# Kernel optimization log

Hardware: AMD Instinct MI355X
Metric: run time of the kernel (lower is better)

Reference implementation:

```python
import jax, jax.numpy as jnp
import numpy as np

NUM_HEADS = 16
HEAD_SIZE = 64
CTXT_LEN = 2048
N_EMBED = 1024
BATCH = 2


def setup_inputs() -> dict:
    key = jax.random.key(0)
    ks = jax.random.split(key, 5)
    s = 0.02  # realistic init scale for weights
    return {
        "x": jax.random.normal(ks[0], (BATCH, CTXT_LEN, N_EMBED), dtype=jnp.float32),
        "Wk": jax.random.normal(ks[1], (N_EMBED, NUM_HEADS * HEAD_SIZE), dtype=jnp.float32) * s,
        "bk": jnp.zeros((NUM_HEADS * HEAD_SIZE,), dtype=jnp.float32),
        "Wq": jax.random.normal(ks[2], (N_EMBED, NUM_HEADS * HEAD_SIZE), dtype=jnp.float32) * s,
        "bq": jnp.zeros((NUM_HEADS * HEAD_SIZE,), dtype=jnp.float32),
        "Wv": jax.random.normal(ks[3], (N_EMBED, NUM_HEADS * HEAD_SIZE), dtype=jnp.float32) * s,
        "bv": jnp.zeros((NUM_HEADS * HEAD_SIZE,), dtype=jnp.float32),
        "Wo": jax.random.normal(ks[4], (NUM_HEADS * HEAD_SIZE, N_EMBED), dtype=jnp.float32) * s,
        "bo": jnp.zeros((N_EMBED,), dtype=jnp.float32),
    }


def reference(x, Wk, bk, Wq, bq, Wv, bv, Wo, bo):
    B, T, E = x.shape
    H, D = NUM_HEADS, HEAD_SIZE
    # QKV projections -> [B, T, H, D]
    k = (x @ Wk + bk).reshape(B, T, H, D)
    q = (x @ Wq + bq).reshape(B, T, H, D)
    v = (x @ Wv + bv).reshape(B, T, H, D)
    # NOTE: source scales by 1/sqrt(n_embed), not 1/sqrt(head_size)
    scale = 1.0 / (E ** 0.5)
    wei = jnp.einsum('bthd,bshd->bhts', q, k) * scale  # [B, H, T, T]
    causal = jnp.tril(jnp.ones((T, T), dtype=bool))
    wei = jnp.where(causal, wei, -jnp.inf)
    wei = jax.nn.softmax(wei, axis=-1)
    # dropout p=0.0 -> identity
    out = jnp.einsum('bhts,bshd->bthd', wei, v).reshape(B, T, H * D)
    return out @ Wo + bo
```

## Files before the change

### kernel.cpp

```cpp
#include <hip/hip_runtime.h>

#define NH 16
#define HS 64
#define T_CTX 2048
#define NE 1024
#define NB 2
#define BT (NB*T_CTX)
#define HD (NH*HS)

typedef unsigned short u16;
typedef __bf16 bf16_t;
typedef bf16_t bf16x8 __attribute__((ext_vector_type(8)));
typedef float f32x4 __attribute__((ext_vector_type(4)));
typedef u16 u16x8 __attribute__((ext_vector_type(8)));
typedef u16 u16x4 __attribute__((ext_vector_type(4)));

#define GLDS(gp, lp) __builtin_amdgcn_global_load_lds( \
    (const __attribute__((address_space(1))) void*)(gp), \
    (__attribute__((address_space(3))) void*)(lp), 16, 0, 0)

__device__ __forceinline__ u16 f2bf(float f) {
  union { float f; unsigned u; } x; x.f = f;
  return (u16)((x.u + 0x7fffu + ((x.u >> 16) & 1u)) >> 16);
}
__device__ __forceinline__ float bf2f(u16 u) {
  union { unsigned u; float f; } x; x.u = ((unsigned)u) << 16;
  return x.f;
}

__global__ __launch_bounds__(256) void k_prep_x(const float* __restrict__ x,
                                                u16* __restrict__ xb) {
  int i = blockIdx.x * blockDim.x + threadIdx.x;
  float4 v = ((const float4*)x)[i];
  ushort4 o;
  o.x = f2bf(v.x); o.y = f2bf(v.y); o.z = f2bf(v.z); o.w = f2bf(v.w);
  ((ushort4*)xb)[i] = o;
}

__global__ __launch_bounds__(256) void k_prep_w(
    const float* __restrict__ W0, const float* __restrict__ W1,
    const float* __restrict__ W2, const float* __restrict__ W3,
    u16* __restrict__ T0, u16* __restrict__ T1,
    u16* __restrict__ T2, u16* __restrict__ T3) {
  const float* W; u16* T;
  switch (blockIdx.z) {
    case 0: W = W0; T = T0; break;
    case 1: W = W1; T = T1; break;
    case 2: W = W2; T = T2; break;
    default: W = W3; T = T3; break;
  }
  __shared__ u16 tile[64 * 72];
  int k0 = blockIdx.x * 64, n0 = blockIdx.y * 64;
  int tid = threadIdx.x;
#pragma unroll
  for (int it = 0; it < 4; ++it) {
    int ci = tid + it * 256;
    int k = ci >> 4, c = ci & 15;
    float4 v = *(const float4*)&W[(size_t)(k0 + k) * NE + n0 + c * 4];
    int n = c * 4;
    tile[(n + 0) * 72 + k] = f2bf(v.x);
    tile[(n + 1) * 72 + k] = f2bf(v.y);
    tile[(n + 2) * 72 + k] = f2bf(v.z);
    tile[(n + 3) * 72 + k] = f2bf(v.w);
  }
  __syncthreads();
#pragma unroll
  for (int it = 0; it < 2; ++it) {
    int co = tid + it * 256;
    int n = co >> 3, c = co & 7;
    u16x8 v = *(const u16x8*)&tile[n * 72 + c * 8];
    *(u16x8*)&T[(size_t)(n0 + n) * NE + k0 + c * 8] = v;
  }
}

__device__ __forceinline__ void gemm_core(
    const u16* __restrict__ A, const u16* __restrict__ Bt,
    int m0, int n0, u16* As, u16* Bs, f32x4 (&acc)[4][4]) {
  const int tid = threadIdx.x, lane = tid & 63, w = tid >> 6;
  const int wm = (w >> 1) * 64, wn = (w & 1) * 64;
  const int q = lane >> 4, l16 = lane & 15;
#pragma unroll
  for (int i = 0; i < 4; ++i)
#pragma unroll
    for (int j = 0; j < 4; ++j)
#pragma unroll
      for (int r = 0; r < 4; ++r) acc[i][j][r] = 0.f;

  for (int k0 = 0; k0 < NE; k0 += 32) {
#pragma unroll
    for (int s2 = 0; s2 < 2; ++s2) {
      int ci = w * 64 + lane + s2 * 256;
      int row = ci >> 2, cc = ci & 3;
      GLDS(A  + (size_t)(m0 + row) * NE + k0 + cc * 8, As + (size_t)(w * 64 + s2 * 256) * 8);
      GLDS(Bt + (size_t)(n0 + row) * NE + k0 + cc * 8, Bs + (size_t)(w * 64 + s2 * 256) * 8);
    }
    __syncthreads();
    bf16x8 av[4], bv4[4];
#pragma unroll
    for (int i = 0; i < 4; ++i) av[i]  = *(const bf16x8*)&As[(wm + i * 16 + l16) * 32 + q * 8];
#pragma unroll
    for (int j = 0; j < 4; ++j) bv4[j] = *(const bf16x8*)&Bs[(wn + j * 16 + l16) * 32 + q * 8];
#pragma unroll
    for (int i = 0; i < 4; ++i)
#pragma unroll
      for (int j = 0; j < 4; ++j)
        acc[i][j] = __builtin_amdgcn_mfma_f32_16x16x32_bf16(av[i], bv4[j], acc[i][j], 0, 0, 0);
    __syncthreads();
  }
}

__global__ __launch_bounds__(256) void k_gemm_qkv(
    const u16* __restrict__ xb, const u16* __restrict__ Wt,
    const float* __restrict__ bq, const float* __restrict__ bk,
    const float* __restrict__ bv, u16* __restrict__ qkv) {
  __shared__ u16 As[128 * 32], Bs[128 * 32];
  const int z = blockIdx.z;
  const u16* W = Wt + (size_t)z * NE * HD;
  const float* bias = (z == 0) ? bq : (z == 1 ? bk : bv);
  u16* dst = qkv + (size_t)z * BT * HD;
  const float scale = (z == 0) ? 0.03125f * 1.4426950408889634f : 1.0f;
  const int m0 = blockIdx.x * 128, n0 = blockIdx.y * 128;
  f32x4 acc[4][4];
  gemm_core(xb, W, m0, n0, As, Bs, acc);
  const int lane = threadIdx.x & 63, w = threadIdx.x >> 6;
  const int wm = (w >> 1) * 64, wn = (w & 1) * 64, q = lane >> 4, l16 = lane & 15;
#pragma unroll
  for (int j = 0; j < 4; ++j) {
    int n = n0 + wn + j * 16 + l16;
    float bn = bias[n];
    int h = n >> 6, d = n & 63;
#pragma unroll
    for (int i = 0; i < 4; ++i)
#pragma unroll
      for (int r = 0; r < 4; ++r) {
        int m = m0 + wm + i * 16 + q * 4 + r;
        int bb = m >> 11, t = m & (T_CTX - 1);
        dst[(((size_t)(bb * NH + h)) * T_CTX + t) * HS + d] =
            f2bf((acc[i][j][r] + bn) * scale);
      }
  }
}

__global__ __launch_bounds__(256) void k_vt(const u16* __restrict__ V,
                                            u16* __restrict__ Vt) {
  int bh = blockIdx.y, t0 = blockIdx.x * 64;
  const u16* src = V + (size_t)bh * T_CTX * HS;
  u16* dst = Vt + (size_t)bh * HS * T_CTX;
  __shared__ u16 tile[64 * 72];
  int tid = threadIdx.x;
#pragma unroll
  for (int it = 0; it < 2; ++it) {
    int ci = tid + it * 256;
    int t = ci >> 3, c = ci & 7;
    u16x8 v = *(const u16x8*)&src[(size_t)(t0 + t) * HS + c * 8];
#pragma unroll
    for (int e = 0; e < 8; ++e) tile[(c * 8 + e) * 72 + t] = v[e];
  }
  __syncthreads();
#pragma unroll
  for (int it = 0; it < 2; ++it) {
    int co = tid + it * 256;
    int d = co >> 3, c = co & 7;
    u16x8 v = *(const u16x8*)&tile[d * 72 + c * 8];
    *(u16x8*)&dst[(size_t)d * T_CTX + t0 + c * 8] = v;
  }
}

__global__ __launch_bounds__(256, 2) void k_attn(
    const u16* __restrict__ Qw, const u16* __restrict__ Kw,
    const u16* __restrict__ Vtw, u16* __restrict__ opart,
    float* __restrict__ ml) {
  __shared__ u16 Ks[128 * 64];
  __shared__ u16 Vs[64 * 128];
  __shared__ u16 Ps[128 * 128];

  const int bh = blockIdx.y;
  const int x = blockIdx.x;
  const int qt = 15 - (x >> 1);
  const int part = x & 1;
  const int n = qt + 1;
  const int half = (n + 1) >> 1;
  const int klo = part ? half : 0;
  const int khi = part ? n : half;
  const int qbase = qt * 128;

  const u16* Qp = Qw + (size_t)bh * T_CTX * HS;
  const u16* Kp = Kw + (size_t)bh * T_CTX * HS;
  const u16* Vp = Vtw + (size_t)bh * HS * T_CTX;

  const int tid = threadIdx.x, lane = tid & 63, w = tid >> 6;
  const int q = lane >> 4, c = lane & 15;
  const int rbase = w * 32;

  bf16x8 aq[2][2];
#pragma unroll
  for (int i = 0; i < 2; ++i)
#pragma unroll
    for (int s = 0; s < 2; ++s)
      aq[i][s] = *(const bf16x8*)&Qp[(size_t)(qbase + rbase + i * 16 + c) * HS + s * 32 + q * 8];

  f32x4 o[2][4];
  float mrow[2], lrow[2];
#pragma unroll
  for (int i = 0; i < 2; ++i) {
    mrow[i] = -__builtin_inff(); lrow[i] = 0.f;
#pragma unroll
    for (int j = 0; j < 4; ++j)
#pragma unroll
      for (int r = 0; r < 4; ++r) o[i][j][r] = 0.f;
  }

  for (int kt = klo; kt < khi; ++kt) {
    const int k0 = kt * 128;
#pragma unroll
    for (int it = 0; it < 4; ++it) {
      int ci = tid + it * 256;
      int row = ci >> 3, cc = ci & 7;
      *(u16x8*)&Ks[row * 64 + (cc ^ (row & 7)) * 8] =
          *(const u16x8*)&Kp[(size_t)(k0 + row) * HS + cc * 8];
      int d = ci >> 4, c2 = ci & 15;
      *(u16x8*)&Vs[d * 128 + (c2 ^ (d & 15)) * 8] =
          *(const u16x8*)&Vp[(size_t)d * T_CTX + k0 + c2 * 8];
    }
    __syncthreads();

    f32x4 s[8][2];
#pragma unroll
    for (int i2 = 0; i2 < 8; ++i2)
#pragma unroll
      for (int j2 = 0; j2 < 2; ++j2)
#pragma unroll
        for (int r = 0; r < 4; ++r) s[i2][j2][r] = 0.f;
#pragma unroll
    for (int i2 = 0; i2 < 8; ++i2) {
      int krow = i2 * 16 + c;
      bf16x8 kf0 = *(const bf16x8*)&Ks[krow * 64 + ((0 + q) ^ (krow & 7)) * 8];
      bf16x8 kf1 = *(const bf16x8*)&Ks[krow * 64 + ((4 + q) ^ (krow & 7)) * 8];
#pragma unroll
      for (int j2 = 0; j2 < 2; ++j2) {
        s[i2][j2] = __builtin_amdgcn_mfma_f32_16x16x32_bf16(kf0, aq[j2][0], s[i2][j2], 0, 0, 0);
        s[i2][j2] = __builtin_amdgcn_mfma_f32_16x16x32_bf16(kf1, aq[j2][1], s[i2][j2], 0, 0, 0);
      }
    }

    if (kt == qt) {
#pragma unroll
      for (int i2 = 0; i2 < 8; ++i2)
#pragma unroll
        for (int j2 = 0; j2 < 2; ++j2)
#pragma unroll
          for (int r = 0; r < 4; ++r) {
            int key = k0 + i2 * 16 + q * 4 + r;
            int qrow = qbase + rbase + j2 * 16 + c;
            if (key > qrow) s[i2][j2][r] = -__builtin_inff();
          }
    }

    float alpha[2];
#pragma unroll
    for (int j2 = 0; j2 < 2; ++j2) {
      float mx = s[0][j2][0];
#pragma unroll
      for (int i2 = 0; i2 < 8; ++i2)
#pragma unroll
        for (int r = 0; r < 4; ++r) mx = fmaxf(mx, s[i2][j2][r]);
      mx = fmaxf(mx, __shfl_xor(mx, 16, 64));
      mx = fmaxf(mx, __shfl_xor(mx, 32, 64));
      float mn = fmaxf(mrow[j2], mx);
      alpha[j2] = __builtin_amdgcn_exp2f(mrow[j2] - mn);
      mrow[j2] = mn;
    }

#pragma unroll
    for (int j2 = 0; j2 < 2; ++j2) {
      const int qrow = rbase + j2 * 16 + c;
      float rs = 0.f;
#pragma unroll
      for (int i2 = 0; i2 < 8; ++i2) {
        u16x4 pk;
#pragma unroll
        for (int r = 0; r < 4; ++r) {
          float p = __builtin_amdgcn_exp2f(s[i2][j2][r] - mrow[j2]);
          rs += p;
          pk[r] = f2bf(p);
        }
        *(u16x4*)&Ps[qrow * 128 + (((i2 * 2 + (q >> 1)) ^ c) * 8) + (q & 1) * 4] = pk;
      }
      rs += __shfl_xor(rs, 16, 64);
      rs += __shfl_xor(rs, 32, 64);
      lrow[j2] = lrow[j2] * alpha[j2] + rs;
    }

#pragma unroll
    for (int i = 0; i < 2; ++i) {
#pragma unroll
      for (int r = 0; r < 4; ++r) {
        float af = __shfl(alpha[i], q * 4 + r, 64);
#pragma unroll
        for (int j = 0; j < 4; ++j) o[i][j][r] *= af;
      }
    }

#pragma unroll
    for (int ks = 0; ks < 4; ++ks) {
      bf16x8 bv4[4];
#pragma unroll
      for (int j = 0; j < 4; ++j) {
        int d = j * 16 + c;
        bv4[j] = *(const bf16x8*)&Vs[d * 128 + (((ks * 4 + q) ^ c) * 8)];
      }
#pragma unroll
      for (int i = 0; i < 2; ++i) {
        int qrow = rbase + i * 16 + c;
        bf16x8 a = *(const bf16x8*)&Ps[qrow * 128 + (((ks * 4 + q) ^ c) * 8)];
#pragma unroll
        for (int j = 0; j < 4; ++j)
          o[i][j] = __builtin_amdgcn_mfma_f32_16x16x32_bf16(a, bv4[j], o[i][j], 0, 0, 0);
      }
    }
    __syncthreads();
  }

  const size_t prow0 = (size_t)(part * 32 + bh) * T_CTX;
  if (q == 0) {
#pragma unroll
    for (int i = 0; i < 2; ++i) {
      size_t t = prow0 + qbase + rbase + i * 16 + c;
      ml[t * 2 + 0] = mrow[i];
      ml[t * 2 + 1] = lrow[i];
    }
  }
#pragma unroll
  for (int i = 0; i < 2; ++i)
#pragma unroll
    for (int r = 0; r < 4; ++r) {
      size_t t = prow0 + qbase + rbase + i * 16 + q * 4 + r;
#pragma unroll
      for (int j = 0; j < 4; ++j)
        opart[t * 64 + j * 16 + c] = f2bf(o[i][j][r]);
    }
}

__global__ __launch_bounds__(256) void k_combine(
    const u16* __restrict__ opart, const float* __restrict__ ml,
    u16* __restrict__ att) {
  int idx = blockIdx.x * 256 + threadIdx.x;
  int row = idx >> 3, oct = idx & 7;
  float m0 = ml[(size_t)row * 2], l0 = ml[(size_t)row * 2 + 1];
  float m1 = ml[((size_t)65536 + row) * 2], l1 = ml[((size_t)65536 + row) * 2 + 1];
  float mm = fmaxf(m0, m1);
  float w0 = __builtin_amdgcn_exp2f(m0 - mm);
  float w1 = __builtin_amdgcn_exp2f(m1 - mm);
  float inv = 1.f / (w0 * l0 + w1 * l1);
  w0 *= inv; w1 *= inv;
  u16x8 a = *(const u16x8*)&opart[(size_t)row * 64 + oct * 8];
  u16x8 b = *(const u16x8*)&opart[(size_t)65536 * 64 + (size_t)row * 64 + oct * 8];
  u16x8 ov;
#pragma unroll
  for (int e = 0; e < 8; ++e) ov[e] = f2bf(w0 * bf2f(a[e]) + w1 * bf2f(b[e]));
  int bh = row >> 11, t = row & 2047, bb = bh >> 4, h = bh & 15;
  *(u16x8*)&att[((size_t)(bb * T_CTX + t)) * HD + h * 64 + oct * 8] = ov;
}

__global__ __launch_bounds__(256) void k_gemm_out(
    const u16* __restrict__ attb, const u16* __restrict__ Wot,
    const float* __restrict__ bo, float* __restrict__ out) {
  __shared__ u16 As[128 * 32], Bs[128 * 32];
  const int m0 = blockIdx.x * 128, n0 = blockIdx.y * 128;
  f32x4 acc[4][4];
  gemm_core(attb, Wot, m0, n0, As, Bs, acc);
  const int lane = threadIdx.x & 63, w = threadIdx.x >> 6;
  const int wm = (w >> 1) * 64, wn = (w & 1) * 64, q = lane >> 4, l16 = lane & 15;
#pragma unroll
  for (int j = 0; j < 4; ++j) {
    int n = n0 + wn + j * 16 + l16;
    float bn = bo[n];
#pragma unroll
    for (int i = 0; i < 4; ++i)
#pragma unroll
      for (int r = 0; r < 4; ++r) {
        int m = m0 + wm + i * 16 + q * 4 + r;
        out[(size_t)m * NE + n] = acc[i][j][r] + bn;
      }
  }
}

extern "C" void kernel_launch(void* const* d_in, const int* in_sizes, int n_in,
                              void* d_out, int out_size, void* d_ws, size_t ws_size,
                              hipStream_t stream) {
  (void)in_sizes; (void)n_in; (void)out_size; (void)ws_size;
  const float* x  = (const float*)d_in[0];
  const float* Wk = (const float*)d_in[1];
  const float* bk = (const float*)d_in[2];
  const float* Wq = (const float*)d_in[3];
  const float* bq = (const float*)d_in[4];
  const float* Wv = (const float*)d_in[5];
  const float* bv = (const float*)d_in[6];
  const float* Wo = (const float*)d_in[7];
  const float* bo = (const float*)d_in[8];
  float* out = (float*)d_out;

  u16* xb    = (u16*)d_ws;
  u16* Wt    = xb  + (size_t)4  * 1024 * 1024;
  u16* Wot   = xb  + (size_t)7  * 1024 * 1024;
  u16* Qw    = xb  + (size_t)8  * 1024 * 1024;
  u16* Kw    = xb  + (size_t)12 * 1024 * 1024;
  u16* Vw    = xb  + (size_t)16 * 1024 * 1024;
  u16* Vtw   = xb  + (size_t)24 * 1024 * 1024;
  u16* opart = Vw;
  float* ml  = (float*)Wt;
  u16* attw  = xb;

  k_prep_x<<<dim3(BT * NE / 4 / 256), 256, 0, stream>>>(x, xb);
  k_prep_w<<<dim3(16, 16, 4), 256, 0, stream>>>(
      Wq, Wk, Wv, Wo, Wt, Wt + (size_t)NE * HD, Wt + (size_t)2 * NE * HD, Wot);
  k_gemm_qkv<<<dim3(32, 8, 3), 256, 0, stream>>>(xb, Wt, bq, bk, bv, Qw);
  k_vt<<<dim3(32, 32), 256, 0, stream>>>(Vw, Vtw);
  k_attn<<<dim3(32, 32), 256, 0, stream>>>(Qw, Kw, Vtw, opart, ml);
  k_combine<<<dim3(2048), 256, 0, stream>>>(opart, ml, attw);
  k_gemm_out<<<dim3(32, 8), 256, 0, stream>>>(attw, Wot, bo, out);
}
```

Measured before the change: 218.4 us.

## Double-buffer attention KV via direct LDS loads, 3-way split, fuse V transpose

The attention kernel now stages 64-key K/V tiles into double-buffered LDS with global_load_lds, overlapping the next tile's load with the current tile's compute. Each query tile's key range is split three ways instead of two (48x32 grid) for better load balance, and the combine kernel merges three partials. The QKV GEMM writes V directly in transposed layout, removing the separate transpose kernel. P is packed to bf16 with a perm-based truncating round, and -1e30 replaces -inf. This trades extra partial output traffic and a larger combine for more parallelism and hidden load latency.

```diff
diff --git a/kernel.cpp b/kernel.cpp
--- a/kernel.cpp
+++ b/kernel.cpp
@@ -26,6 +26,10 @@
 __device__ __forceinline__ float bf2f(u16 u) {
   union { unsigned u; float f; } x; x.u = ((unsigned)u) << 16;
   return x.f;
+}
+__device__ __forceinline__ unsigned pack_bf2(float hi, float lo) {
+  union { float f; unsigned u; } H, L; H.f = hi; L.f = lo;
+  return __builtin_amdgcn_perm(H.u + 0x8000u, L.u + 0x8000u, 0x07060302);
 }
 
 __global__ __launch_bounds__(256) void k_prep_x(const float* __restrict__ x,
@@ -112,76 +116,84 @@
 __global__ __launch_bounds__(256) void k_gemm_qkv(
     const u16* __restrict__ xb, const u16* __restrict__ Wt,
     const float* __restrict__ bq, const float* __restrict__ bk,
-    const float* __restrict__ bv, u16* __restrict__ qkv) {
+    const float* __restrict__ bv, u16* __restrict__ Qw,
+    u16* __restrict__ Kw, u16* __restrict__ Vtw) {
   __shared__ u16 As[128 * 32], Bs[128 * 32];
   const int z = blockIdx.z;
   const u16* W = Wt + (size_t)z * NE * HD;
   const float* bias = (z == 0) ? bq : (z == 1 ? bk : bv);
-  u16* dst = qkv + (size_t)z * BT * HD;
   const float scale = (z == 0) ? 0.03125f * 1.4426950408889634f : 1.0f;
   const int m0 = blockIdx.x * 128, n0 = blockIdx.y * 128;
   f32x4 acc[4][4];
   gemm_core(xb, W, m0, n0, As, Bs, acc);
   const int lane = threadIdx.x & 63, w = threadIdx.x >> 6;
   const int wm = (w >> 1) * 64, wn = (w & 1) * 64, q = lane >> 4, l16 = lane & 15;
-#pragma unroll
-  for (int j = 0; j < 4; ++j) {
-    int n = n0 + wn + j * 16 + l16;
-    float bn = bias[n];
-    int h = n >> 6, d = n & 63;
-#pragma unroll
-    for (int i = 0; i < 4; ++i)
-#pragma unroll
-      for (int r = 0; r < 4; ++r) {
-        int m = m0 + wm + i * 16 + q * 4 + r;
-        int bb = m >> 11, t = m & (T_CTX - 1);
-        dst[(((size_t)(bb * NH + h)) * T_CTX + t) * HS + d] =
-            f2bf((acc[i][j][r] + bn) * scale);
-      }
-  }
-}
-
-__global__ __launch_bounds__(256) void k_vt(const u16* __restrict__ V,
-                                            u16* __restrict__ Vt) {
-  int bh = blockIdx.y, t0 = blockIdx.x * 64;
-  const u16* src = V + (size_t)bh * T_CTX * HS;
-  u16* dst = Vt + (size_t)bh * HS * T_CTX;
-  __shared__ u16 tile[64 * 72];
-  int tid = threadIdx.x;
+  if (z == 2) {
+#pragma unroll
+    for (int j = 0; j < 4; ++j) {
+      int n = n0 + wn + j * 16 + l16;
+      float bn = bias[n];
+      int h = n >> 6, d = n & 63;
+#pragma unroll
+      for (int i = 0; i < 4; ++i) {
+        int m = m0 + wm + i * 16 + q * 4;
+        int bb = m >> 11, t0 = m & (T_CTX - 1);
+        u16x4 pk;
+#pragma unroll
+        for (int r = 0; r < 4; ++r) pk[r] = f2bf(acc[i][j][r] + bn);
+        *(u16x4*)&Vtw[((size_t)((bb * NH + h) * HS + d)) * T_CTX + t0] = pk;
+      }
+    }
+  } else {
+    u16* dst = (z == 0) ? Qw : Kw;
+#pragma unroll
+    for (int j = 0; j < 4; ++j) {
+      int n = n0 + wn + j * 16 + l16;
+      float bn = bias[n];
+      int h = n >> 6, d = n & 63;
+#pragma unroll
+      for (int i = 0; i < 4; ++i)
+#pragma unroll
+        for (int r = 0; r < 4; ++r) {
+          int m = m0 + wm + i * 16 + q * 4 + r;
+          int bb = m >> 11, t = m & (T_CTX - 1);
+          dst[(((size_t)(bb * NH + h)) * T_CTX + t) * HS + d] =
+              f2bf((acc[i][j][r] + bn) * scale);
+        }
+    }
+  }
+}
+
+__device__ __forceinline__ void stage_kv(const u16* __restrict__ Kp,
+                                         const u16* __restrict__ Vp,
+                                         int k0, u16* KsB, u16* VsB, int tid) {
 #pragma unroll
   for (int it = 0; it < 2; ++it) {
     int ci = tid + it * 256;
-    int t = ci >> 3, c = ci & 7;
-    u16x8 v = *(const u16x8*)&src[(size_t)(t0 + t) * HS + c * 8];
-#pragma unroll
-    for (int e = 0; e < 8; ++e) tile[(c * 8 + e) * 72 + t] = v[e];
-  }
-  __syncthreads();
-#pragma unroll
-  for (int it = 0; it < 2; ++it) {
-    int co = tid + it * 256;
-    int d = co >> 3, c = co & 7;
-    u16x8 v = *(const u16x8*)&tile[d * 72 + c * 8];
-    *(u16x8*)&dst[(size_t)d * T_CTX + t0 + c * 8] = v;
-  }
-}
-
-__global__ __launch_bounds__(256, 2) void k_attn(
+    int row = ci >> 3, cc = ci & 7;
+    int sw = (cc ^ (row & 7)) * 8;
+    GLDS(Kp + (size_t)(k0 + row) * HS + sw, KsB + ci * 8);
+    GLDS(Vp + (size_t)row * T_CTX + k0 + sw, VsB + ci * 8);
+  }
+}
+
+__global__ __launch_bounds__(256) void k_attn(
     const u16* __restrict__ Qw, const u16* __restrict__ Kw,
-    const u16* __restrict__ Vtw, u16* __restrict__ opart,
+    const u16* __restrict__ Vtw, u16* __restrict__ op0,
+    u16* __restrict__ op1, u16* __restrict__ op2,
     float* __restrict__ ml) {
-  __shared__ u16 Ks[128 * 64];
-  __shared__ u16 Vs[64 * 128];
-  __shared__ u16 Ps[128 * 128];
+  __shared__ u16 Ks[2 * 64 * 64];
+  __shared__ u16 Vs[2 * 64 * 64];
+  __shared__ u16 Ps[128 * 64];
 
   const int bh = blockIdx.y;
   const int x = blockIdx.x;
-  const int qt = 15 - (x >> 1);
-  const int part = x & 1;
-  const int n = qt + 1;
-  const int half = (n + 1) >> 1;
-  const int klo = part ? half : 0;
-  const int khi = part ? n : half;
+  const int qt = 15 - x / 3;
+  const int part = x - (15 - qt) * 3;
+  const int ntiles = 2 * (qt + 1);
+  const int npt = (ntiles + 2) / 3;
+  const int klo = part * npt;
+  const int khi = min(klo + npt, ntiles);
   const int qbase = qt * 128;
 
   const u16* Qp = Qw + (size_t)bh * T_CTX * HS;
@@ -203,56 +215,48 @@
   float mrow[2], lrow[2];
 #pragma unroll
   for (int i = 0; i < 2; ++i) {
-    mrow[i] = -__builtin_inff(); lrow[i] = 0.f;
+    mrow[i] = -1e30f; lrow[i] = 0.f;
 #pragma unroll
     for (int j = 0; j < 4; ++j)
 #pragma unroll
       for (int r = 0; r < 4; ++r) o[i][j][r] = 0.f;
   }
 
+  if (klo < khi) stage_kv(Kp, Vp, klo * 64, Ks, Vs, tid);
+
   for (int kt = klo; kt < khi; ++kt) {
-    const int k0 = kt * 128;
-#pragma unroll
-    for (int it = 0; it < 4; ++it) {
-      int ci = tid + it * 256;
-      int row = ci >> 3, cc = ci & 7;
-      *(u16x8*)&Ks[row * 64 + (cc ^ (row & 7)) * 8] =
-          *(const u16x8*)&Kp[(size_t)(k0 + row) * HS + cc * 8];
-      int d = ci >> 4, c2 = ci & 15;
-      *(u16x8*)&Vs[d * 128 + (c2 ^ (d & 15)) * 8] =
-          *(const u16x8*)&Vp[(size_t)d * T_CTX + k0 + c2 * 8];
-    }
+    const int k0 = kt * 64;
+    const int buf = (kt - klo) & 1;
+    u16* KsB = Ks + buf * 4096;
+    u16* VsB = Vs + buf * 4096;
     __syncthreads();
-
-    f32x4 s[8][2];
-#pragma unroll
-    for (int i2 = 0; i2 < 8; ++i2)
-#pragma unroll
-      for (int j2 = 0; j2 < 2; ++j2)
-#pragma unroll
-        for (int r = 0; r < 4; ++r) s[i2][j2][r] = 0.f;
-#pragma unroll
-    for (int i2 = 0; i2 < 8; ++i2) {
+    if (kt + 1 < khi)
+      stage_kv(Kp, Vp, k0 + 64, Ks + (buf ^ 1) * 4096, Vs + (buf ^ 1) * 4096, tid);
+
+    f32x4 s[4][2];
+#pragma unroll
+    for (int i2 = 0; i2 < 4; ++i2) {
       int krow = i2 * 16 + c;
-      bf16x8 kf0 = *(const bf16x8*)&Ks[krow * 64 + ((0 + q) ^ (krow & 7)) * 8];
-      bf16x8 kf1 = *(const bf16x8*)&Ks[krow * 64 + ((4 + q) ^ (krow & 7)) * 8];
+      bf16x8 kf0 = *(const bf16x8*)&KsB[krow * 64 + ((0 + q) ^ (krow & 7)) * 8];
+      bf16x8 kf1 = *(const bf16x8*)&KsB[krow * 64 + ((4 + q) ^ (krow & 7)) * 8];
 #pragma unroll
       for (int j2 = 0; j2 < 2; ++j2) {
-        s[i2][j2] = __builtin_amdgcn_mfma_f32_16x16x32_bf16(kf0, aq[j2][0], s[i2][j2], 0, 0, 0);
-        s[i2][j2] = __builtin_amdgcn_mfma_f32_16x16x32_bf16(kf1, aq[j2][1], s[i2][j2], 0, 0, 0);
-      }
-    }
-
-    if (kt == qt) {
-#pragma unroll
-      for (int i2 = 0; i2 < 8; ++i2)
+        f32x4 z4 = {0.f, 0.f, 0.f, 0.f};
+        z4 = __builtin_amdgcn_mfma_f32_16x16x32_bf16(kf0, aq[j2][0], z4, 0, 0, 0);
+        s[i2][j2] = __builtin_amdgcn_mfma_f32_16x16x32_bf16(kf1, aq[j2][1], z4, 0, 0, 0);
+      }
+    }
+
+    if (k0 + 63 > qbase + rbase) {
+#pragma unroll
+      for (int i2 = 0; i2 < 4; ++i2)
 #pragma unroll
         for (int j2 = 0; j2 < 2; ++j2)
 #pragma unroll
           for (int r = 0; r < 4; ++r) {
             int key = k0 + i2 * 16 + q * 4 + r;
             int qrow = qbase + rbase + j2 * 16 + c;
-            if (key > qrow) s[i2][j2][r] = -__builtin_inff();
+            if (key > qrow) s[i2][j2][r] = -1e30f;
           }
     }
 
@@ -261,7 +265,7 @@
     for (int j2 = 0; j2 < 2; ++j2) {
       float mx = s[0][j2][0];
 #pragma unroll
-      for (int i2 = 0; i2 < 8; ++i2)
+      for (int i2 = 0; i2 < 4; ++i2)
 #pragma unroll
         for (int r = 0; r < 4; ++r) mx = fmaxf(mx, s[i2][j2][r]);
       mx = fmaxf(mx, __shfl_xor(mx, 16, 64));
@@ -276,15 +280,17 @@
       const int qrow = rbase + j2 * 16 + c;
       float rs = 0.f;
 #pragma unroll
-      for (int i2 = 0; i2 < 8; ++i2) {
-        u16x4 pk;
+      for (int i2 = 0; i2 < 4; ++i2) {
+        float p[4];
 #pragma unroll
         for (int r = 0; r < 4; ++r) {
-          float p = __builtin_amdgcn_exp2f(s[i2][j2][r] - mrow[j2]);
-          rs += p;
-          pk[r] = f2bf(p);
+          p[r] = __builtin_amdgcn_exp2f(s[i2][j2][r] - mrow[j2]);
+          rs += p[r];
         }
-        *(u16x4*)&Ps[qrow * 128 + (((i2 * 2 + (q >> 1)) ^ c) * 8) + (q & 1) * 4] = pk;
+        uint2 pd;
+        pd.x = pack_bf2(p[1], p[0]);
+        pd.y = pack_bf2(p[3], p[2]);
+        *(uint2*)&Ps[qrow * 64 + ((i2 * 2 + (q >> 1)) ^ (c & 7)) * 8 + (q & 1) * 4] = pd;
       }
       rs += __shfl_xor(rs, 16, 64);
       rs += __shfl_xor(rs, 32, 64);
@@ -302,30 +308,30 @@
     }
 
 #pragma unroll
-    for (int ks = 0; ks < 4; ++ks) {
+    for (int ks = 0; ks < 2; ++ks) {
       bf16x8 bv4[4];
 #pragma unroll
       for (int j = 0; j < 4; ++j) {
         int d = j * 16 + c;
-        bv4[j] = *(const bf16x8*)&Vs[d * 128 + (((ks * 4 + q) ^ c) * 8)];
+        bv4[j] = *(const bf16x8*)&VsB[d * 64 + ((ks * 4 + q) ^ (d & 7)) * 8];
       }
 #pragma unroll
       for (int i = 0; i < 2; ++i) {
         int qrow = rbase + i * 16 + c;
-        bf16x8 a = *(const bf16x8*)&Ps[qrow * 128 + (((ks * 4 + q) ^ c) * 8)];
+        bf16x8 a = *(const bf16x8*)&Ps[qrow * 64 + ((ks * 4 + q) ^ (c & 7)) * 8];
 #pragma unroll
         for (int j = 0; j < 4; ++j)
           o[i][j] = __builtin_amdgcn_mfma_f32_16x16x32_bf16(a, bv4[j], o[i][j], 0, 0, 0);
       }
     }
-    __syncthreads();
-  }
-
-  const size_t prow0 = (size_t)(part * 32 + bh) * T_CTX;
+  }
+
+  u16* op = (part == 0) ? op0 : (part == 1 ? op1 : op2);
+  const size_t row0 = (size_t)bh * T_CTX + qbase;
   if (q == 0) {
 #pragma unroll
     for (int i = 0; i < 2; ++i) {
-      size_t t = prow0 + qbase + rbase + i * 16 + c;
+      size_t t = (size_t)part * 65536 + row0 + rbase + i * 16 + c;
       ml[t * 2 + 0] = mrow[i];
       ml[t * 2 + 1] = lrow[i];
     }
@@ -334,30 +340,35 @@
   for (int i = 0; i < 2; ++i)
 #pragma unroll
     for (int r = 0; r < 4; ++r) {
-      size_t t = prow0 + qbase + rbase + i * 16 + q * 4 + r;
+      size_t t = row0 + rbase + i * 16 + q * 4 + r;
 #pragma unroll
       for (int j = 0; j < 4; ++j)
-        opart[t * 64 + j * 16 + c] = f2bf(o[i][j][r]);
+        op[t * 64 + j * 16 + c] = f2bf(o[i][j][r]);
     }
 }
 
 __global__ __launch_bounds__(256) void k_combine(
-    const u16* __restrict__ opart, const float* __restrict__ ml,
+    const u16* __restrict__ op0, const u16* __restrict__ op1,
+    const u16* __restrict__ op2, const float* __restrict__ ml,
     u16* __restrict__ att) {
   int idx = blockIdx.x * 256 + threadIdx.x;
   int row = idx >> 3, oct = idx & 7;
-  float m0 = ml[(size_t)row * 2], l0 = ml[(size_t)row * 2 + 1];
-  float m1 = ml[((size_t)65536 + row) * 2], l1 = ml[((size_t)65536 + row) * 2 + 1];
-  float mm = fmaxf(m0, m1);
+  float m0 = ml[(size_t)row * 2],                  l0 = ml[(size_t)row * 2 + 1];
+  float m1 = ml[((size_t)65536 + row) * 2],        l1 = ml[((size_t)65536 + row) * 2 + 1];
+  float m2 = ml[((size_t)131072 + row) * 2],       l2 = ml[((size_t)131072 + row) * 2 + 1];
+  float mm = fmaxf(m0, fmaxf(m1, m2));
   float w0 = __builtin_amdgcn_exp2f(m0 - mm);
   float w1 = __builtin_amdgcn_exp2f(m1 - mm);
-  float inv = 1.f / (w0 * l0 + w1 * l1);
-  w0 *= inv; w1 *= inv;
-  u16x8 a = *(const u16x8*)&opart[(size_t)row * 64 + oct * 8];
-  u16x8 b = *(const u16x8*)&opart[(size_t)65536 * 64 + (size_t)row * 64 + oct * 8];
+  float w2 = __builtin_amdgcn_exp2f(m2 - mm);
+  float inv = 1.f / (w0 * l0 + w1 * l1 + w2 * l2);
+  w0 *= inv; w1 *= inv; w2 *= inv;
+  u16x8 a = *(const u16x8*)&op0[(size_t)row * 64 + oct * 8];
+  u16x8 b = *(const u16x8*)&op1[(size_t)row * 64 + oct * 8];
+  u16x8 d = *(const u16x8*)&op2[(size_t)row * 64 + oct * 8];
   u16x8 ov;
 #pragma unroll
-  for (int e = 0; e < 8; ++e) ov[e] = f2bf(w0 * bf2f(a[e]) + w1 * bf2f(b[e]));
+  for (int e = 0; e < 8; ++e)
+    ov[e] = f2bf(w0 * bf2f(a[e]) + w1 * bf2f(b[e]) + w2 * bf2f(d[e]));
   int bh = row >> 11, t = row & 2047, bb = bh >> 4, h = bh & 15;
   *(u16x8*)&att[((size_t)(bb * T_CTX + t)) * HD + h * 64 + oct * 8] = ov;
 }
@@ -400,23 +411,25 @@
   const float* bo = (const float*)d_in[8];
   float* out = (float*)d_out;
 
-  u16* xb    = (u16*)d_ws;
-  u16* Wt    = xb  + (size_t)4  * 1024 * 1024;
-  u16* Wot   = xb  + (size_t)7  * 1024 * 1024;
-  u16* Qw    = xb  + (size_t)8  * 1024 * 1024;
-  u16* Kw    = xb  + (size_t)12 * 1024 * 1024;
-  u16* Vw    = xb  + (size_t)16 * 1024 * 1024;
-  u16* Vtw   = xb  + (size_t)24 * 1024 * 1024;
-  u16* opart = Vw;
-  float* ml  = (float*)Wt;
-  u16* attw  = xb;
+  u16* base = (u16*)d_ws;
+  const size_t M = 1024 * 1024;
+  u16* xb   = base;
+  u16* Wt   = base + 4 * M;
+  u16* Wot  = base + 7 * M;
+  u16* Qw   = base + 8 * M;
+  u16* Kw   = base + 12 * M;
+  u16* Vtw  = base + 16 * M;
+  u16* op0  = base + 20 * M;
+  u16* op1  = base + 24 * M;
+  u16* op2  = base;
+  float* ml = (float*)(base + 4 * M);
+  u16* attw = base + 12 * M;
 
   k_prep_x<<<dim3(BT * NE / 4 / 256), 256, 0, stream>>>(x, xb);
   k_prep_w<<<dim3(16, 16, 4), 256, 0, stream>>>(
       Wq, Wk, Wv, Wo, Wt, Wt + (size_t)NE * HD, Wt + (size_t)2 * NE * HD, Wot);
-  k_gemm_qkv<<<dim3(32, 8, 3), 256, 0, stream>>>(xb, Wt, bq, bk, bv, Qw);
-  k_vt<<<dim3(32, 32), 256, 0, stream>>>(Vw, Vtw);
-  k_attn<<<dim3(32, 32), 256, 0, stream>>>(Qw, Kw, Vtw, opart, ml);
-  k_combine<<<dim3(2048), 256, 0, stream>>>(opart, ml, attw);
+  k_gemm_qkv<<<dim3(32, 8, 3), 256, 0, stream>>>(xb, Wt, bq, bk, bv, Qw, Kw, Vtw);
+  k_attn<<<dim3(48, 32), 256, 0, stream>>>(Qw, Kw, Vtw, op0, op1, op2, ml);
+  k_combine<<<dim3(2048), 256, 0, stream>>>(op0, op1, op2, ml, attw);
   k_gemm_out<<<dim3(32, 8), 256, 0, stream>>>(attw, Wot, bo, out);
 }
```

New measurement: 232.6 us. 1.06x slower.
